# Kernel tuning notes

Hardware: AMD Instinct MI355X
Metric: run time of the kernel (lower is better)

Reference implementation:

```python
import jax, jax.numpy as jnp
import numpy as np

EMBED_DIM = 1024
NUM_HEADS = 16
HEAD_DIM = EMBED_DIM // NUM_HEADS
BATCH = 2
SEQ = 2048


def setup_inputs() -> dict:
    key = jax.random.key(0)
    k_x, k_wqkv, k_bqkv, k_wo, k_bo = jax.random.split(key, 5)
    scale = 1.0 / np.sqrt(EMBED_DIM)
    return {
        "x": jax.random.normal(k_x, (BATCH, SEQ, EMBED_DIM), dtype=jnp.float32),
        # torch nn.Linear stores weight as (out, in); we keep (in, out) and use x @ W
        "W_qkv": jax.random.normal(k_wqkv, (EMBED_DIM, 3 * EMBED_DIM), dtype=jnp.float32) * scale,
        "b_qkv": jax.random.normal(k_bqkv, (3 * EMBED_DIM,), dtype=jnp.float32) * scale,
        "W_out": jax.random.normal(k_wo, (EMBED_DIM, EMBED_DIM), dtype=jnp.float32) * scale,
        "b_out": jax.random.normal(k_bo, (EMBED_DIM,), dtype=jnp.float32) * scale,
    }


def reference(x, W_qkv, b_qkv, W_out, b_out):
    B, S, E = x.shape
    qkv = x @ W_qkv + b_qkv                                   # (B,S,3E)
    qkv = qkv.reshape(B, S, 3, NUM_HEADS, HEAD_DIM)
    qkv = jnp.transpose(qkv, (2, 0, 3, 1, 4))                  # (3,B,H,S,D)
    Q, K, V = qkv[0], qkv[1], qkv[2]
    scores = jnp.einsum("bhqd,bhkd->bhqk", Q, K) / np.sqrt(HEAD_DIM)
    causal = jnp.tril(jnp.ones((S, S), dtype=bool))
    scores = jnp.where(causal[None, None], scores, -jnp.inf)
    attention_weights = jax.nn.softmax(scores, axis=-1)        # (B,H,S,S)
    # dropout is identity in eval mode
    attended = jnp.einsum("bhqk,bhkd->bhqd", attention_weights, V)
    attended = jnp.transpose(attended, (0, 2, 1, 3)).reshape(B, S, E)
    output = attended @ W_out + b_out
    return output, attention_weights
```

## Files before the change

kernel.cpp:

```cpp
#include <hip/hip_runtime.h>
#include <hip/hip_bf16.h>
#include <math.h>

#define BATCH 2
#define SEQ 2048
#define EMBED 1024
#define NHEAD 16
#define QKV_N 3072
#define M_TOK 4096
#define OUT_ELEMS ((size_t)M_TOK * EMBED)

typedef __attribute__((ext_vector_type(4))) float f32x4;
typedef __attribute__((ext_vector_type(8))) short bf16x8;

__device__ __forceinline__ short f2bf(float f) {
    __hip_bfloat16 h = __float2bfloat16(f);
    return *reinterpret_cast<short*>(&h);
}

__device__ __forceinline__ void gld16(const void* g, void* l) {
    __builtin_amdgcn_global_load_lds(
        (const __attribute__((address_space(1))) unsigned int*)g,
        (__attribute__((address_space(3))) unsigned int*)l, 16, 0, 0);
}

__global__ __launch_bounds__(256) void cast_bf16_kernel(
    const float* __restrict__ in, short* __restrict__ out, int n4)
{
    int i = blockIdx.x * 256 + threadIdx.x;
    if (i >= n4) return;
    float4 v = ((const float4*)in)[i];
    unsigned long long pk =
        (unsigned long long)(unsigned short)f2bf(v.x)
      | ((unsigned long long)(unsigned short)f2bf(v.y) << 16)
      | ((unsigned long long)(unsigned short)f2bf(v.z) << 32)
      | ((unsigned long long)(unsigned short)f2bf(v.w) << 48);
    ((unsigned long long*)out)[i] = pk;
}

__global__ __launch_bounds__(256) void transpose_cast_kernel(
    const float* __restrict__ in, short* __restrict__ out, int R, int C)
{
    __shared__ float t[64][65];
    const int r0 = blockIdx.y * 64, c0 = blockIdx.x * 64;
    for (int i = threadIdx.x; i < 4096; i += 256) {
        int r = i >> 6, c = i & 63;
        t[r][c] = in[(size_t)(r0 + r) * C + c0 + c];
    }
    __syncthreads();
    for (int i = threadIdx.x; i < 4096; i += 256) {
        int c = i >> 6, r = i & 63;
        out[(size_t)(c0 + c) * R + r0 + r] = f2bf(t[r][c]);
    }
}

template <bool OUT_BF16>
__global__ __launch_bounds__(256) void gemm_mfma_kernel(
    const short* __restrict__ A, const short* __restrict__ Bt,
    const float* __restrict__ bias, void* __restrict__ C,
    int M, int N, int K)
{
    __shared__ short As[128 * 32];
    __shared__ short Bs[128 * 32];
    const int tid = threadIdx.x;
    const int w = tid >> 6, lane = tid & 63;
    const int quad = lane >> 4, lc = lane & 15;
    const int wm = w & 1, wn = w >> 1;
    const int m0 = blockIdx.y * 128, n0 = blockIdx.x * 128;

    f32x4 acc[4][4] = {};

    const int srow = (lane >> 2);
    const int skp = (lane & 3) * 8;

    for (int k0 = 0; k0 < K; k0 += 32) {
        #pragma unroll
        for (int j = 0; j < 2; ++j) {
            int r = w * 32 + j * 16 + srow;
            gld16(A + ((size_t)(m0 + r) * K + k0 + skp), &As[(w * 32 + j * 16) * 32]);
            gld16(Bt + ((size_t)(n0 + r) * K + k0 + skp), &Bs[(w * 32 + j * 16) * 32]);
        }
        __syncthreads();
        bf16x8 af[4], bf[4];
        #pragma unroll
        for (int i = 0; i < 4; ++i)
            af[i] = *(const bf16x8*)&As[(wm * 64 + i * 16 + lc) * 32 + quad * 8];
        #pragma unroll
        for (int i = 0; i < 4; ++i)
            bf[i] = *(const bf16x8*)&Bs[(wn * 64 + i * 16 + lc) * 32 + quad * 8];
        #pragma unroll
        for (int mi = 0; mi < 4; ++mi)
            #pragma unroll
            for (int ni = 0; ni < 4; ++ni)
                acc[mi][ni] = __builtin_amdgcn_mfma_f32_16x16x32_bf16(
                    af[mi], bf[ni], acc[mi][ni], 0, 0, 0);
        __syncthreads();
    }

    #pragma unroll
    for (int mi = 0; mi < 4; ++mi) {
        int row = m0 + wm * 64 + mi * 16 + quad * 4;
        #pragma unroll
        for (int ni = 0; ni < 4; ++ni) {
            int col = n0 + wn * 64 + ni * 16 + lc;
            float bc = bias[col];
            #pragma unroll
            for (int r = 0; r < 4; ++r) {
                float v = acc[mi][ni][r] + bc;
                if (OUT_BF16)
                    ((short*)C)[(size_t)(row + r) * N + col] = f2bf(v);
                else
                    ((float*)C)[(size_t)(row + r) * N + col] = v;
            }
        }
    }
}

__global__ __launch_bounds__(256) void attn_kernel(
    const short* __restrict__ qkvb,
    float* __restrict__ attw,
    short* __restrict__ attb)
{
    const int qt = gridDim.x - 1 - blockIdx.x;
    const int bh = blockIdx.y;
    const int b = bh >> 4, h = bh & 15;
    const int tid = threadIdx.x;
    const int w = tid >> 6, lane = tid & 63;
    const int quad = lane >> 4, lc = lane & 15;
    const int qloc = w * 16 + quad * 4;

    __shared__ short Kb[64 * 64];
    __shared__ short Vt[64 * 72];
    __shared__ short Ps[4][16 * 72];

    const short* qptr = qkvb + (size_t)(b * SEQ + qt * 64 + w * 16 + lc) * QKV_N
                        + h * 64 + quad * 8;
    const bf16x8 qf0 = *(const bf16x8*)qptr;
    const bf16x8 qf1 = *(const bf16x8*)(qptr + 32);

    float m_i[4], l_i[4];
    #pragma unroll
    for (int r = 0; r < 4; ++r) { m_i[r] = -INFINITY; l_i[r] = 0.f; }

    for (int kt = 0; kt <= qt; ++kt) {
        __syncthreads();
        #pragma unroll
        for (int j = 0; j < 2; ++j) {
            int row = w * 16 + j * 8 + (lane >> 3);
            const short* g = qkvb + (size_t)(b * SEQ + kt * 64 + row) * QKV_N
                             + EMBED + h * 64 + (lane & 7) * 8;
            gld16(g, &Kb[(w * 16 + j * 8) * 64]);
        }
        __syncthreads();

        const bool diag = (kt == qt);
        float sv[4][4];
        #pragma unroll
        for (int ni = 0; ni < 4; ++ni) {
            f32x4 acc = 0;
            bf16x8 kf0 = *(const bf16x8*)&Kb[(ni * 16 + lc) * 64 + quad * 8];
            bf16x8 kf1 = *(const bf16x8*)&Kb[(ni * 16 + lc) * 64 + 32 + quad * 8];
            acc = __builtin_amdgcn_mfma_f32_16x16x32_bf16(qf0, kf0, acc, 0, 0, 0);
            acc = __builtin_amdgcn_mfma_f32_16x16x32_bf16(qf1, kf1, acc, 0, 0, 0);
            #pragma unroll
            for (int r = 0; r < 4; ++r) {
                float v = acc[r] * 0.125f;
                if (diag && (ni * 16 + lc) > (qloc + r)) v = -INFINITY;
                sv[ni][r] = v;
            }
        }
        #pragma unroll
        for (int r = 0; r < 4; ++r) {
            float mx = fmaxf(fmaxf(sv[0][r], sv[1][r]), fmaxf(sv[2][r], sv[3][r]));
            #pragma unroll
            for (int d = 1; d <= 8; d <<= 1) mx = fmaxf(mx, __shfl_xor(mx, d, 64));
            float mn = fmaxf(m_i[r], mx);
            float s = __expf(sv[0][r] - mn) + __expf(sv[1][r] - mn)
                    + __expf(sv[2][r] - mn) + __expf(sv[3][r] - mn);
            #pragma unroll
            for (int d = 1; d <= 8; d <<= 1) s += __shfl_xor(s, d, 64);
            l_i[r] = l_i[r] * __expf(m_i[r] - mn) + s;
            m_i[r] = mn;
        }
    }

    float inv_l[4];
    #pragma unroll
    for (int r = 0; r < 4; ++r) inv_l[r] = 1.0f / l_i[r];

    f32x4 o[4] = {};
    for (int kt = 0; kt <= qt; ++kt) {
        __syncthreads();
        #pragma unroll
        for (int j = 0; j < 2; ++j) {
            int row = w * 16 + j * 8 + (lane >> 3);
            const short* g = qkvb + (size_t)(b * SEQ + kt * 64 + row) * QKV_N
                             + EMBED + h * 64 + (lane & 7) * 8;
            gld16(g, &Kb[(w * 16 + j * 8) * 64]);
        }
        {
            int key = tid & 63, dg = tid >> 6;
            const short* vs = qkvb + (size_t)(b * SEQ + kt * 64 + key) * QKV_N
                              + 2 * EMBED + h * 64 + dg * 16;
            bf16x8 v0 = *(const bf16x8*)vs;
            bf16x8 v1 = *(const bf16x8*)(vs + 8);
            #pragma unroll
            for (int jj = 0; jj < 8; ++jj) {
                Vt[(dg * 16 + jj) * 72 + key] = v0[jj];
                Vt[(dg * 16 + 8 + jj) * 72 + key] = v1[jj];
            }
        }
        __syncthreads();

        const bool diag = (kt == qt);
        short* Psw = Ps[w];
        #pragma unroll
        for (int ni = 0; ni < 4; ++ni) {
            f32x4 acc = 0;
            bf16x8 kf0 = *(const bf16x8*)&Kb[(ni * 16 + lc) * 64 + quad * 8];
            bf16x8 kf1 = *(const bf16x8*)&Kb[(ni * 16 + lc) * 64 + 32 + quad * 8];
            acc = __builtin_amdgcn_mfma_f32_16x16x32_bf16(qf0, kf0, acc, 0, 0, 0);
            acc = __builtin_amdgcn_mfma_f32_16x16x32_bf16(qf1, kf1, acc, 0, 0, 0);
            #pragma unroll
            for (int r = 0; r < 4; ++r) {
                float v = acc[r] * 0.125f;
                bool msk = diag && (ni * 16 + lc) > (qloc + r);
                float p = msk ? 0.f : __expf(v - m_i[r]) * inv_l[r];
                attw[((size_t)bh * SEQ + qt * 64 + qloc + r) * SEQ
                     + kt * 64 + ni * 16 + lc] = p;
                Psw[(quad * 4 + r) * 72 + ni * 16 + lc] = f2bf(p);
            }
        }
        #pragma unroll
        for (int kd = 0; kd < 2; ++kd) {
            bf16x8 pf = *(const bf16x8*)&Psw[lc * 72 + kd * 32 + quad * 8];
            #pragma unroll
            for (int ni = 0; ni < 4; ++ni) {
                bf16x8 vf = *(const bf16x8*)&Vt[(ni * 16 + lc) * 72 + kd * 32 + quad * 8];
                o[ni] = __builtin_amdgcn_mfma_f32_16x16x32_bf16(pf, vf, o[ni], 0, 0, 0);
            }
        }
    }

    #pragma unroll
    for (int ni = 0; ni < 4; ++ni)
        #pragma unroll
        for (int r = 0; r < 4; ++r)
            attb[(size_t)(b * SEQ + qt * 64 + qloc + r) * EMBED
                 + h * 64 + ni * 16 + lc] = f2bf(o[ni][r]);

    if (qt < (int)gridDim.x - 1) {
        const int zc4 = (qt + 1) * 16;
        for (int r = 0; r < 64; ++r) {
            f32x4* rowp = (f32x4*)(attw + ((size_t)bh * SEQ + qt * 64 + r) * SEQ);
            for (int c = zc4 + tid; c < 512; c += 256) rowp[c] = 0;
        }
    }
}

extern "C" void kernel_launch(void* const* d_in, const int* in_sizes, int n_in,
                              void* d_out, int out_size, void* d_ws, size_t ws_size,
                              hipStream_t stream)
{
    const float* x     = (const float*)d_in[0];
    const float* W_qkv = (const float*)d_in[1];
    const float* b_qkv = (const float*)d_in[2];
    const float* W_out = (const float*)d_in[3];
    const float* b_out = (const float*)d_in[4];

    float* out  = (float*)d_out;
    float* attw = out + OUT_ELEMS;

    short* xb   = (short*)d_ws;
    short* wqt  = xb + (size_t)M_TOK * EMBED;
    short* wot  = wqt + (size_t)QKV_N * EMBED;
    short* qkvb = wot + (size_t)EMBED * EMBED;
    short* attb = qkvb + (size_t)M_TOK * QKV_N;

    cast_bf16_kernel<<<OUT_ELEMS / 4 / 256, 256, 0, stream>>>(x, xb, (int)(OUT_ELEMS / 4));
    transpose_cast_kernel<<<dim3(QKV_N / 64, EMBED / 64), 256, 0, stream>>>(W_qkv, wqt, EMBED, QKV_N);
    transpose_cast_kernel<<<dim3(EMBED / 64, EMBED / 64), 256, 0, stream>>>(W_out, wot, EMBED, EMBED);

    gemm_mfma_kernel<true><<<dim3(QKV_N / 128, M_TOK / 128), 256, 0, stream>>>(
        xb, wqt, b_qkv, qkvb, M_TOK, QKV_N, EMBED);

    attn_kernel<<<dim3(SEQ / 64, BATCH * NHEAD), 256, 0, stream>>>(qkvb, attw, attb);

    gemm_mfma_kernel<false><<<dim3(EMBED / 128, M_TOK / 128), 256, 0, stream>>>(
        attb, wot, b_out, out, M_TOK, EMBED, EMBED);
}
```

Before: 799.3 us.

## Pre-pack V, swizzle LDS tiles, vectorize nontemporal attention-weight stores

Adds a kernel that transposes V into per-tile, XOR-swizzled blocks so the attention kernel can load V with direct global-to-LDS copies instead of scalar transposing stores. The GEMM, K, V and P shared-memory tiles use XOR swizzles in place of padding to avoid bank conflicts. Attention weights are written as 16-byte nontemporal rows read back from the bf16 P tile, replacing scattered scalar fp32 stores. Query tiles are also interleaved across heads for load balance. The stored attention weights now go through bf16 rounding, which loses precision, and the change adds an extra kernel launch plus a pass over V.

After: 772.5 us. -3.4%, faster.

```diff
diff --git a/kernel.cpp b/kernel.cpp
--- a/kernel.cpp
+++ b/kernel.cpp
@@ -8,6 +8,7 @@
 #define NHEAD 16
 #define QKV_N 3072
 #define M_TOK 4096
+#define NT_KV (SEQ / 64)
 #define OUT_ELEMS ((size_t)M_TOK * EMBED)
 
 typedef __attribute__((ext_vector_type(4))) float f32x4;
@@ -16,6 +17,11 @@
 __device__ __forceinline__ short f2bf(float f) {
     __hip_bfloat16 h = __float2bfloat16(f);
     return *reinterpret_cast<short*>(&h);
+}
+__device__ __forceinline__ float bf2f(short s) {
+    union { unsigned u; float f; } c;
+    c.u = ((unsigned)(unsigned short)s) << 16;
+    return c.f;
 }
 
 __device__ __forceinline__ void gld16(const void* g, void* l) {
@@ -54,6 +60,36 @@
     }
 }
 
+__global__ __launch_bounds__(256) void pack_v_kernel(
+    const short* __restrict__ qkvb, short* __restrict__ Vp)
+{
+    __shared__ short tv[64][72];
+    const int kt = blockIdx.x, bh = blockIdx.y;
+    const int b = bh >> 4, h = bh & 15;
+    const int t = threadIdx.x;
+    const int row = t >> 2, cp = t & 3;
+    const short* src = qkvb + (size_t)(b * SEQ + kt * 64 + row) * QKV_N
+                       + 2 * EMBED + h * 64 + cp * 16;
+    bf16x8 a0 = *(const bf16x8*)src;
+    bf16x8 a1 = *(const bf16x8*)(src + 8);
+    #pragma unroll
+    for (int j = 0; j < 8; ++j) {
+        tv[row][cp * 16 + j] = a0[j];
+        tv[row][cp * 16 + 8 + j] = a1[j];
+    }
+    __syncthreads();
+    const int d = row;
+    short* dst = Vp + ((size_t)bh * NT_KV + kt) * 4096 + d * 64;
+    bf16x8 o0, o1;
+    #pragma unroll
+    for (int j = 0; j < 8; ++j) {
+        o0[j] = tv[cp * 16 + j][d];
+        o1[j] = tv[cp * 16 + 8 + j][d];
+    }
+    *(bf16x8*)(dst + (((2 * cp) ^ (d & 7)) << 3)) = o0;
+    *(bf16x8*)(dst + (((2 * cp + 1) ^ (d & 7)) << 3)) = o1;
+}
+
 template <bool OUT_BF16>
 __global__ __launch_bounds__(256) void gemm_mfma_kernel(
     const short* __restrict__ A, const short* __restrict__ Bt,
@@ -71,23 +107,25 @@
     f32x4 acc[4][4] = {};
 
     const int srow = (lane >> 2);
-    const int skp = (lane & 3) * 8;
+    const int schk = ((lane & 3) ^ (srow & 3)) * 8;
 
     for (int k0 = 0; k0 < K; k0 += 32) {
         #pragma unroll
         for (int j = 0; j < 2; ++j) {
             int r = w * 32 + j * 16 + srow;
-            gld16(A + ((size_t)(m0 + r) * K + k0 + skp), &As[(w * 32 + j * 16) * 32]);
-            gld16(Bt + ((size_t)(n0 + r) * K + k0 + skp), &Bs[(w * 32 + j * 16) * 32]);
+            gld16(A + ((size_t)(m0 + r) * K + k0 + schk), &As[(w * 32 + j * 16) * 32]);
+            gld16(Bt + ((size_t)(n0 + r) * K + k0 + schk), &Bs[(w * 32 + j * 16) * 32]);
         }
         __syncthreads();
         bf16x8 af[4], bf[4];
         #pragma unroll
         for (int i = 0; i < 4; ++i)
-            af[i] = *(const bf16x8*)&As[(wm * 64 + i * 16 + lc) * 32 + quad * 8];
+            af[i] = *(const bf16x8*)&As[(wm * 64 + i * 16 + lc) * 32
+                                        + ((quad ^ (lc & 3)) << 3)];
         #pragma unroll
         for (int i = 0; i < 4; ++i)
-            bf[i] = *(const bf16x8*)&Bs[(wn * 64 + i * 16 + lc) * 32 + quad * 8];
+            bf[i] = *(const bf16x8*)&Bs[(wn * 64 + i * 16 + lc) * 32
+                                        + ((quad ^ (lc & 3)) << 3)];
         #pragma unroll
         for (int mi = 0; mi < 4; ++mi)
             #pragma unroll
@@ -118,10 +156,12 @@
 
 __global__ __launch_bounds__(256) void attn_kernel(
     const short* __restrict__ qkvb,
+    const short* __restrict__ Vp,
     float* __restrict__ attw,
     short* __restrict__ attb)
 {
-    const int qt = gridDim.x - 1 - blockIdx.x;
+    const int NT = NT_KV;
+    const int qt = (blockIdx.y & 8) ? (NT - 1 - (int)blockIdx.x) : (int)blockIdx.x;
     const int bh = blockIdx.y;
     const int b = bh >> 4, h = bh & 15;
     const int tid = threadIdx.x;
@@ -130,14 +170,17 @@
     const int qloc = w * 16 + quad * 4;
 
     __shared__ short Kb[64 * 64];
-    __shared__ short Vt[64 * 72];
-    __shared__ short Ps[4][16 * 72];
+    __shared__ short Vt[64 * 64];
+    __shared__ short Ps[4][16 * 64];
 
     const short* qptr = qkvb + (size_t)(b * SEQ + qt * 64 + w * 16 + lc) * QKV_N
                         + h * 64 + quad * 8;
     const bf16x8 qf0 = *(const bf16x8*)qptr;
     const bf16x8 qf1 = *(const bf16x8*)(qptr + 32);
 
+    const int srow = lane >> 3;
+    const int schk = ((lane & 7) ^ srow) * 8;
+
     float m_i[4], l_i[4];
     #pragma unroll
     for (int r = 0; r < 4; ++r) { m_i[r] = -INFINITY; l_i[r] = 0.f; }
@@ -146,10 +189,10 @@
         __syncthreads();
         #pragma unroll
         for (int j = 0; j < 2; ++j) {
-            int row = w * 16 + j * 8 + (lane >> 3);
-            const short* g = qkvb + (size_t)(b * SEQ + kt * 64 + row) * QKV_N
-                             + EMBED + h * 64 + (lane & 7) * 8;
-            gld16(g, &Kb[(w * 16 + j * 8) * 64]);
+            int row = w * 16 + j * 8 + srow;
+            gld16(qkvb + (size_t)(b * SEQ + kt * 64 + row) * QKV_N
+                       + EMBED + h * 64 + schk,
+                  &Kb[(w * 16 + j * 8) * 64]);
         }
         __syncthreads();
 
@@ -157,15 +200,16 @@
         float sv[4][4];
         #pragma unroll
         for (int ni = 0; ni < 4; ++ni) {
-            f32x4 acc = 0;
-            bf16x8 kf0 = *(const bf16x8*)&Kb[(ni * 16 + lc) * 64 + quad * 8];
-            bf16x8 kf1 = *(const bf16x8*)&Kb[(ni * 16 + lc) * 64 + 32 + quad * 8];
+            const int key = ni * 16 + lc;
+            f32x4 acc = {};
+            bf16x8 kf0 = *(const bf16x8*)&Kb[key * 64 + ((quad ^ (key & 7)) << 3)];
+            bf16x8 kf1 = *(const bf16x8*)&Kb[key * 64 + (((quad | 4) ^ (key & 7)) << 3)];
             acc = __builtin_amdgcn_mfma_f32_16x16x32_bf16(qf0, kf0, acc, 0, 0, 0);
             acc = __builtin_amdgcn_mfma_f32_16x16x32_bf16(qf1, kf1, acc, 0, 0, 0);
             #pragma unroll
             for (int r = 0; r < 4; ++r) {
                 float v = acc[r] * 0.125f;
-                if (diag && (ni * 16 + lc) > (qloc + r)) v = -INFINITY;
+                if (diag && key > (qloc + r)) v = -INFINITY;
                 sv[ni][r] = v;
             }
         }
@@ -193,22 +237,12 @@
         __syncthreads();
         #pragma unroll
         for (int j = 0; j < 2; ++j) {
-            int row = w * 16 + j * 8 + (lane >> 3);
-            const short* g = qkvb + (size_t)(b * SEQ + kt * 64 + row) * QKV_N
-                             + EMBED + h * 64 + (lane & 7) * 8;
-            gld16(g, &Kb[(w * 16 + j * 8) * 64]);
-        }
-        {
-            int key = tid & 63, dg = tid >> 6;
-            const short* vs = qkvb + (size_t)(b * SEQ + kt * 64 + key) * QKV_N
-                              + 2 * EMBED + h * 64 + dg * 16;
-            bf16x8 v0 = *(const bf16x8*)vs;
-            bf16x8 v1 = *(const bf16x8*)(vs + 8);
-            #pragma unroll
-            for (int jj = 0; jj < 8; ++jj) {
-                Vt[(dg * 16 + jj) * 72 + key] = v0[jj];
-                Vt[(dg * 16 + 8 + jj) * 72 + key] = v1[jj];
-            }
+            int row = w * 16 + j * 8 + srow;
+            gld16(qkvb + (size_t)(b * SEQ + kt * 64 + row) * QKV_N
+                       + EMBED + h * 64 + schk,
+                  &Kb[(w * 16 + j * 8) * 64]);
+            gld16(Vp + ((size_t)bh * NT + kt) * 4096 + (w * 16 + j * 8) * 64 + lane * 8,
+                  &Vt[(w * 16 + j * 8) * 64]);
         }
         __syncthreads();
 
@@ -216,28 +250,46 @@
         short* Psw = Ps[w];
         #pragma unroll
         for (int ni = 0; ni < 4; ++ni) {
-            f32x4 acc = 0;
-            bf16x8 kf0 = *(const bf16x8*)&Kb[(ni * 16 + lc) * 64 + quad * 8];
-            bf16x8 kf1 = *(const bf16x8*)&Kb[(ni * 16 + lc) * 64 + 32 + quad * 8];
+            const int key = ni * 16 + lc;
+            f32x4 acc = {};
+            bf16x8 kf0 = *(const bf16x8*)&Kb[key * 64 + ((quad ^ (key & 7)) << 3)];
+            bf16x8 kf1 = *(const bf16x8*)&Kb[key * 64 + (((quad | 4) ^ (key & 7)) << 3)];
             acc = __builtin_amdgcn_mfma_f32_16x16x32_bf16(qf0, kf0, acc, 0, 0, 0);
             acc = __builtin_amdgcn_mfma_f32_16x16x32_bf16(qf1, kf1, acc, 0, 0, 0);
             #pragma unroll
             for (int r = 0; r < 4; ++r) {
                 float v = acc[r] * 0.125f;
-                bool msk = diag && (ni * 16 + lc) > (qloc + r);
+                bool msk = diag && key > (qloc + r);
                 float p = msk ? 0.f : __expf(v - m_i[r]) * inv_l[r];
-                attw[((size_t)bh * SEQ + qt * 64 + qloc + r) * SEQ
-                     + kt * 64 + ni * 16 + lc] = p;
-                Psw[(quad * 4 + r) * 72 + ni * 16 + lc] = f2bf(p);
+                int prow = quad * 4 + r;
+                Psw[prow * 64 + (key ^ ((prow & 7) << 3))] = f2bf(p);
             }
         }
         #pragma unroll
         for (int kd = 0; kd < 2; ++kd) {
-            bf16x8 pf = *(const bf16x8*)&Psw[lc * 72 + kd * 32 + quad * 8];
+            bf16x8 pf = *(const bf16x8*)&Psw[lc * 64
+                        + (((kd * 4 + quad) ^ (lc & 7)) << 3)];
             #pragma unroll
             for (int ni = 0; ni < 4; ++ni) {
-                bf16x8 vf = *(const bf16x8*)&Vt[(ni * 16 + lc) * 72 + kd * 32 + quad * 8];
+                const int d = ni * 16 + lc;
+                bf16x8 vf = *(const bf16x8*)&Vt[d * 64
+                            + (((kd * 4 + quad) ^ (d & 7)) << 3)];
                 o[ni] = __builtin_amdgcn_mfma_f32_16x16x32_bf16(pf, vf, o[ni], 0, 0, 0);
+            }
+        }
+        {
+            const int a = lane & 7;
+            #pragma unroll
+            for (int wb = 0; wb < 2; ++wb) {
+                const int r8 = wb * 8 + srow;
+                bf16x8 pv = *(const bf16x8*)&Psw[r8 * 64 + a * 8];
+                const int colc = (a ^ (r8 & 7)) << 3;
+                float* dst = attw + ((size_t)bh * SEQ + qt * 64 + w * 16 + r8) * SEQ
+                             + kt * 64 + colc;
+                f32x4 f0 = { bf2f(pv[0]), bf2f(pv[1]), bf2f(pv[2]), bf2f(pv[3]) };
+                f32x4 f1 = { bf2f(pv[4]), bf2f(pv[5]), bf2f(pv[6]), bf2f(pv[7]) };
+                __builtin_nontemporal_store(f0, (f32x4*)dst);
+                __builtin_nontemporal_store(f1, (f32x4*)dst + 1);
             }
         }
     }
@@ -249,11 +301,13 @@
             attb[(size_t)(b * SEQ + qt * 64 + qloc + r) * EMBED
                  + h * 64 + ni * 16 + lc] = f2bf(o[ni][r]);
 
-    if (qt < (int)gridDim.x - 1) {
+    if (qt < NT - 1) {
         const int zc4 = (qt + 1) * 16;
         for (int r = 0; r < 64; ++r) {
             f32x4* rowp = (f32x4*)(attw + ((size_t)bh * SEQ + qt * 64 + r) * SEQ);
-            for (int c = zc4 + tid; c < 512; c += 256) rowp[c] = 0;
+            f32x4 z = {};
+            for (int c = zc4 + tid; c < 512; c += 256)
+                __builtin_nontemporal_store(z, rowp + c);
         }
     }
 }
@@ -276,6 +330,7 @@
     short* wot  = wqt + (size_t)QKV_N * EMBED;
     short* qkvb = wot + (size_t)EMBED * EMBED;
     short* attb = qkvb + (size_t)M_TOK * QKV_N;
+    short* Vp   = xb;
 
     cast_bf16_kernel<<<OUT_ELEMS / 4 / 256, 256, 0, stream>>>(x, xb, (int)(OUT_ELEMS / 4));
     transpose_cast_kernel<<<dim3(QKV_N / 64, EMBED / 64), 256, 0, stream>>>(W_qkv, wqt, EMBED, QKV_N);
@@ -284,7 +339,9 @@
     gemm_mfma_kernel<true><<<dim3(QKV_N / 128, M_TOK / 128), 256, 0, stream>>>(
         xb, wqt, b_qkv, qkvb, M_TOK, QKV_N, EMBED);
 
-    attn_kernel<<<dim3(SEQ / 64, BATCH * NHEAD), 256, 0, stream>>>(qkvb, attw, attb);
+    pack_v_kernel<<<dim3(NT_KV, BATCH * NHEAD), 256, 0, stream>>>(qkvb, Vp);
+
+    attn_kernel<<<dim3(NT_KV, BATCH * NHEAD), 256, 0, stream>>>(qkvb, Vp, attw, attb);
 
     gemm_mfma_kernel<false><<<dim3(EMBED / 128, M_TOK / 128), 256, 0, stream>>>(
         attb, wot, b_out, out, M_TOK, EMBED, EMBED);
```
